# Optimization experiments

Measured on AMD Instinct MI355X. Metric: run time of the kernel, lower is better.

The kernel has to match this reference:

```python
import jax, jax.numpy as jnp
import numpy as np

jax.config.update("jax_enable_x64", True)  # hash uses int64 multiply-xor like torch .long()

NUM_LEVELS = 16
LEVEL_DIM = 2
PER_LEVEL_SCALE = 2
BASE_RES = 16
LOG2_HASHMAP = 19
PS1 = 19349663  # second spatial hash prime (ps[0] == 1)
N_POINTS = 524288


def _isprime(n):
    for p in range(2, int(n ** 0.5) + 1):
        if n % p == 0:
            return False
    return True


N_ENTRIES = 2 ** LOG2_HASHMAP
while not _isprime(N_ENTRIES):
    N_ENTRIES += 1  # -> 524309

SCALES = []
OFFSETS = [0]
START_HASH = NUM_LEVELS  # module uses -1 sentinel; NUM_LEVELS == 'no hashing yet'
for i in range(NUM_LEVELS):
    res = int(BASE_RES * PER_LEVEL_SCALE ** i)
    SCALES.append(res)
    n = (res + 1) ** 2
    if n > N_ENTRIES:
        if START_HASH == NUM_LEVELS:
            START_HASH = i
        n = N_ENTRIES
    OFFSETS.append(OFFSETS[-1] + n)
TABLE_SIZE = OFFSETS[-1]  # 5594552

CORNERS = jnp.array([[0.0, 0.0], [0.0, 1.0], [1.0, 0.0], [1.0, 1.0]], dtype=jnp.float32)  # [4,2]
SCALES_F = jnp.array(SCALES, dtype=jnp.float32)          # [L]
SCALES_I = jnp.array(SCALES, dtype=jnp.int64)            # [L]
LEVEL_OFF = jnp.array(OFFSETS[:-1], dtype=jnp.int64)     # [L] base offset per level


def setup_inputs() -> dict:
    key = jax.random.key(0)
    k1, k2 = jax.random.split(key)
    x = jax.random.uniform(k1, (N_POINTS, 2), dtype=jnp.float32)  # coords in [0,1)
    data = (jax.random.uniform(k2, (TABLE_SIZE, LEVEL_DIM), dtype=jnp.float32) * 2.0 - 1.0) * 1e-4
    return {"x": x, "data": data}


def reference(x, data):
    L, F = NUM_LEVELS, LEVEL_DIM
    float_x = x[None] * SCALES_F[:, None, None]                                  # [L,N,2]
    int_x = (float_x[:, :, None, :] + CORNERS[None, None]).astype(jnp.int64)     # [L,N,4,2]
    offset_x = float_x - int_x[:, :, 0].astype(float_x.dtype)                    # [L,N,2] frac part
    ix0, ix1 = int_x[..., 0], int_x[..., 1]
    # dense-grid index for low levels, spatial hash for high levels
    grid_ind = ix0 * (SCALES_I + 1)[:, None, None] + ix1                         # [L,N,4]
    hash_ind = (ix0 ^ (ix1 * PS1)) % N_ENTRIES                                   # [L,N,4]
    is_grid = (jnp.arange(L) < START_HASH)[:, None, None]
    ind = jnp.where(is_grid, grid_ind, hash_ind) + LEVEL_OFF[:, None, None]      # [L,N,4]
    val = data[ind]                                                              # [L,N,4,F]
    # bilinear corner weights: clamp(1 - c + (2c-1)*frac) per axis, product over xy
    w = jnp.clip(1.0 - CORNERS[None, None] + (2.0 * CORNERS[None, None] - 1.0) * offset_x[:, :, None], 0.0, 1.0)
    w = w[..., 0] * w[..., 1]                                                    # [L,N,4]
    out = jnp.einsum('lnc,lncf->lnf', w, val)                                    # [L,N,F]
    return out.transpose(1, 0, 2).reshape(-1, L * F)                             # [N, L*F]
```

## Files before the change

kernel.cpp:

```cpp
#include <hip/hip_runtime.h>


static constexpr int  kPoints    = 524288;
static constexpr int  kLevels    = 16;
static constexpr int  kStartHash = 6;
static constexpr unsigned kPs1     = 19349663u;
static constexpr unsigned kEntries = 524309u;
static constexpr unsigned kR32     = 352277u;

__constant__ unsigned c_level_off[kLevels] = {
    0u, 289u, 1378u, 5603u, 22244u, 88293u, 351462u,
    875771u, 1400080u, 1924389u, 2448698u, 2973007u,
    3497316u, 4021625u, 4545934u, 5070243u
};

__device__ __forceinline__ float2 interp_level(
    const float2 p, const float2* __restrict__ tbl, const int l)
{
    const int   scale_i = 16 << l;
    const float scale_f = (float)scale_i;

    const float fx = p.x * scale_f;
    const float fy = p.y * scale_f;

    const unsigned ix0 = (unsigned)(int)fx;
    const unsigned iy0 = (unsigned)(int)fy;
    const unsigned ix1 = (unsigned)(int)(fx + 1.0f);
    const unsigned iy1 = (unsigned)(int)(fy + 1.0f);

    const float ox = fx - (float)ix0;
    const float oy = fy - (float)iy0;

    const float wx1 = fminf(fmaxf(ox, 0.0f), 1.0f);
    const float wx0 = fminf(fmaxf(1.0f - ox, 0.0f), 1.0f);
    const float wy1 = fminf(fmaxf(oy, 0.0f), 1.0f);
    const float wy0 = fminf(fmaxf(1.0f - oy, 0.0f), 1.0f);

    unsigned i00, i01, i10, i11;
    if (l < kStartHash) {
        const unsigned stride = (unsigned)(scale_i + 1);
        i00 = ix0 * stride + iy0;
        i01 = ix0 * stride + iy1;
        i10 = ix1 * stride + iy0;
        i11 = ix1 * stride + iy1;
    } else {
        const unsigned long long hy0 = (unsigned long long)iy0 * kPs1;
        const unsigned long long hy1 = (unsigned long long)iy1 * kPs1;
        const unsigned lo0 = (unsigned)hy0, hi0 = (unsigned)(hy0 >> 32);
        const unsigned lo1 = (unsigned)hy1, hi1 = (unsigned)(hy1 >> 32);
        const unsigned a0 = (hi0 * kR32) % kEntries;
        const unsigned a1 = (hi1 * kR32) % kEntries;
        i00 = a0 + ((lo0 ^ ix0) % kEntries); if (i00 >= kEntries) i00 -= kEntries;
        i01 = a1 + ((lo1 ^ ix0) % kEntries); if (i01 >= kEntries) i01 -= kEntries;
        i10 = a0 + ((lo0 ^ ix1) % kEntries); if (i10 >= kEntries) i10 -= kEntries;
        i11 = a1 + ((lo1 ^ ix1) % kEntries); if (i11 >= kEntries) i11 -= kEntries;
    }

    const unsigned base = c_level_off[l];
    const float2 v00 = tbl[base + i00];
    const float2 v01 = tbl[base + i01];
    const float2 v10 = tbl[base + i10];
    const float2 v11 = tbl[base + i11];

    const float w00 = wx0 * wy0;
    const float w01 = wx0 * wy1;
    const float w10 = wx1 * wy0;
    const float w11 = wx1 * wy1;

    return make_float2(
        w00 * v00.x + w01 * v01.x + w10 * v10.x + w11 * v11.x,
        w00 * v00.y + w01 * v01.y + w10 * v10.y + w11 * v11.y);
}

__global__ __launch_bounds__(256) void level_pass(
    const float2* __restrict__ x,
    const float2* __restrict__ tbl,
    float2* __restrict__ ws)
{
    const int b    = blockIdx.x;
    const int xcd  = b & 7;
    const int slot = b >> 3;

    int level, pblk;
    if (slot < 2048) {
        level = 6 + xcd;
        pblk  = slot;
    } else if (slot < 2304) {
        level = 14;
        pblk  = xcd * 256 + (slot - 2048);
    } else if (slot < 2560) {
        level = 15;
        pblk  = xcd * 256 + (slot - 2304);
    } else {
        const int d = xcd * 1536 + (slot - 2560);
        level = d >> 11;
        pblk  = d & 2047;
    }

    const int n = (pblk << 8) | threadIdx.x;
    const float2 p = x[n];
    ws[((size_t)pblk << 12) + (level << 8) + threadIdx.x] =
        interp_level(p, tbl, level);
}

static constexpr int kTStride = 257;

__global__ __launch_bounds__(256) void transpose_out(
    const float2* __restrict__ ws,
    float4* __restrict__ out)
{
    __shared__ float2 lds[kLevels * kTStride];

    const int t = threadIdx.x;
    const float2* __restrict__ tile = ws + ((size_t)blockIdx.x << 12);

#pragma unroll
    for (int l = 0; l < kLevels; ++l)
        lds[l * kTStride + t] = tile[(l << 8) + t];

    __syncthreads();

    float4* o = out + ((size_t)blockIdx.x << 11);
#pragma unroll
    for (int k = 0; k < 8; ++k) {
        const int f  = k * 256 + t;
        const int nl = f >> 3;
        const int i  = t & 7;
        const float2 a = lds[(2 * i)     * kTStride + nl];
        const float2 b = lds[(2 * i + 1) * kTStride + nl];
        o[f] = make_float4(a.x, a.y, b.x, b.y);
    }
}

__global__ __launch_bounds__(256) void hashgrid_fwd(
    const float2* __restrict__ x,
    const float2* __restrict__ tbl,
    float4* __restrict__ out)
{
    const int n = blockIdx.x * blockDim.x + threadIdx.x;
    if (n >= kPoints) return;
    const float2 p = x[n];
    float acc[2 * kLevels];
#pragma unroll
    for (int l = 0; l < kLevels; ++l) {
        const float2 r = interp_level(p, tbl, l);
        acc[2 * l + 0] = r.x;
        acc[2 * l + 1] = r.y;
    }
    float4* o = out + (size_t)n * 8;
#pragma unroll
    for (int i = 0; i < 8; ++i)
        o[i] = make_float4(acc[4 * i + 0], acc[4 * i + 1],
                           acc[4 * i + 2], acc[4 * i + 3]);
}

extern "C" void kernel_launch(void* const* d_in, const int* in_sizes, int n_in,
                              void* d_out, int out_size, void* d_ws, size_t ws_size,
                              hipStream_t stream) {
    const float2* x   = (const float2*)d_in[0];
    const float2* tbl = (const float2*)d_in[1];

    const size_t ws_needed = (size_t)kLevels * kPoints * sizeof(float2);
    if (ws_size >= ws_needed) {
        float2* ws = (float2*)d_ws;
        level_pass<<<kLevels * (kPoints / 256), 256, 0, stream>>>(x, tbl, ws);
        transpose_out<<<kPoints / 256, 256, 0, stream>>>(ws, (float4*)d_out);
    } else {
        hashgrid_fwd<<<kPoints / 256, 256, 0, stream>>>(x, tbl, (float4*)d_out);
    }
}
```

Measured before the change: 222.6 us.

## Process two points per thread in level pass and use nontemporal workspace accesses

Each level_pass thread now handles two points, computing both corner sets before issuing all eight table gathers so more memory loads are in flight per thread, and the grid is halved accordingly with the XCD-to-level mapping rescaled. Workspace writes, workspace reads in the transpose, and the final output stores use nontemporal builtins to keep streaming data from evicting the hash table out of cache. The trade-off is higher register use and fewer blocks, which may reduce occupancy.

```diff
diff --git a/kernel.cpp b/kernel.cpp
--- a/kernel.cpp
+++ b/kernel.cpp
@@ -8,14 +8,34 @@
 static constexpr unsigned kEntries = 524309u;
 static constexpr unsigned kR32     = 352277u;
 
+typedef float v2f __attribute__((ext_vector_type(2)));
+typedef float v4f __attribute__((ext_vector_type(4)));
+
+__device__ __forceinline__ void nt_store2(float2* p, const float2 v) {
+    v2f t; t.x = v.x; t.y = v.y;
+    __builtin_nontemporal_store(t, (v2f*)p);
+}
+__device__ __forceinline__ float2 nt_load2(const float2* p) {
+    const v2f t = __builtin_nontemporal_load((const v2f*)p);
+    return make_float2(t.x, t.y);
+}
+__device__ __forceinline__ void nt_store4(float4* p, const float4 v) {
+    v4f t; t.x = v.x; t.y = v.y; t.z = v.z; t.w = v.w;
+    __builtin_nontemporal_store(t, (v4f*)p);
+}
+
 __constant__ unsigned c_level_off[kLevels] = {
     0u, 289u, 1378u, 5603u, 22244u, 88293u, 351462u,
     875771u, 1400080u, 1924389u, 2448698u, 2973007u,
     3497316u, 4021625u, 4545934u, 5070243u
 };
 
-__device__ __forceinline__ float2 interp_level(
-    const float2 p, const float2* __restrict__ tbl, const int l)
+struct Corners {
+    float    w00, w01, w10, w11;
+    unsigned i00, i01, i10, i11;
+};
+
+__device__ __forceinline__ Corners prep_level(const float2 p, const int l)
 {
     const int   scale_i = 16 << l;
     const float scale_f = (float)scale_i;
@@ -56,20 +76,25 @@
         i11 = a1 + ((lo1 ^ ix1) % kEntries); if (i11 >= kEntries) i11 -= kEntries;
     }
 
+    Corners c;
     const unsigned base = c_level_off[l];
-    const float2 v00 = tbl[base + i00];
-    const float2 v01 = tbl[base + i01];
-    const float2 v10 = tbl[base + i10];
-    const float2 v11 = tbl[base + i11];
-
-    const float w00 = wx0 * wy0;
-    const float w01 = wx0 * wy1;
-    const float w10 = wx1 * wy0;
-    const float w11 = wx1 * wy1;
-
+    c.i00 = base + i00; c.i01 = base + i01;
+    c.i10 = base + i10; c.i11 = base + i11;
+    c.w00 = wx0 * wy0;  c.w01 = wx0 * wy1;
+    c.w10 = wx1 * wy0;  c.w11 = wx1 * wy1;
+    return c;
+}
+
+__device__ __forceinline__ float2 finish_level(
+    const Corners& c, const float2* __restrict__ tbl)
+{
+    const float2 v00 = tbl[c.i00];
+    const float2 v01 = tbl[c.i01];
+    const float2 v10 = tbl[c.i10];
+    const float2 v11 = tbl[c.i11];
     return make_float2(
-        w00 * v00.x + w01 * v01.x + w10 * v10.x + w11 * v11.x,
-        w00 * v00.y + w01 * v01.y + w10 * v10.y + w11 * v11.y);
+        c.w00 * v00.x + c.w01 * v01.x + c.w10 * v10.x + c.w11 * v11.x,
+        c.w00 * v00.y + c.w01 * v01.y + c.w10 * v10.y + c.w11 * v11.y);
 }
 
 __global__ __launch_bounds__(256) void level_pass(
@@ -82,25 +107,44 @@
     const int slot = b >> 3;
 
     int level, pblk;
-    if (slot < 2048) {
+    if (slot < 1024) {
         level = 6 + xcd;
         pblk  = slot;
-    } else if (slot < 2304) {
+    } else if (slot < 1152) {
         level = 14;
-        pblk  = xcd * 256 + (slot - 2048);
-    } else if (slot < 2560) {
+        pblk  = xcd * 128 + (slot - 1024);
+    } else if (slot < 1280) {
         level = 15;
-        pblk  = xcd * 256 + (slot - 2304);
+        pblk  = xcd * 128 + (slot - 1152);
     } else {
-        const int d = xcd * 1536 + (slot - 2560);
-        level = d >> 11;
-        pblk  = d & 2047;
-    }
-
-    const int n = (pblk << 8) | threadIdx.x;
-    const float2 p = x[n];
-    ws[((size_t)pblk << 12) + (level << 8) + threadIdx.x] =
-        interp_level(p, tbl, level);
+        const int d = xcd * 768 + (slot - 1280);
+        level = d >> 10;
+        pblk  = d & 1023;
+    }
+
+    const int n0 = (pblk << 9) | threadIdx.x;
+    const int n1 = n0 + 256;
+    const float2 pA = x[n0];
+    const float2 pB = x[n1];
+
+    const Corners cA = prep_level(pA, level);
+    const Corners cB = prep_level(pB, level);
+
+    const float2 a00 = tbl[cA.i00], a01 = tbl[cA.i01];
+    const float2 a10 = tbl[cA.i10], a11 = tbl[cA.i11];
+    const float2 b00 = tbl[cB.i00], b01 = tbl[cB.i01];
+    const float2 b10 = tbl[cB.i10], b11 = tbl[cB.i11];
+
+    const float2 rA = make_float2(
+        cA.w00 * a00.x + cA.w01 * a01.x + cA.w10 * a10.x + cA.w11 * a11.x,
+        cA.w00 * a00.y + cA.w01 * a01.y + cA.w10 * a10.y + cA.w11 * a11.y);
+    const float2 rB = make_float2(
+        cB.w00 * b00.x + cB.w01 * b01.x + cB.w10 * b10.x + cB.w11 * b11.x,
+        cB.w00 * b00.y + cB.w01 * b01.y + cB.w10 * b10.y + cB.w11 * b11.y);
+
+    const size_t tile0 = (size_t)(n0 >> 8);
+    nt_store2(&ws[(tile0 << 12) + (level << 8) + (n0 & 255)], rA);
+    nt_store2(&ws[((tile0 + 1) << 12) + (level << 8) + (n1 & 255)], rB);
 }
 
 static constexpr int kTStride = 257;
@@ -116,7 +160,7 @@
 
 #pragma unroll
     for (int l = 0; l < kLevels; ++l)
-        lds[l * kTStride + t] = tile[(l << 8) + t];
+        lds[l * kTStride + t] = nt_load2(&tile[(l << 8) + t]);
 
     __syncthreads();
 
@@ -128,7 +172,7 @@
         const int i  = t & 7;
         const float2 a = lds[(2 * i)     * kTStride + nl];
         const float2 b = lds[(2 * i + 1) * kTStride + nl];
-        o[f] = make_float4(a.x, a.y, b.x, b.y);
+        nt_store4(&o[f], make_float4(a.x, a.y, b.x, b.y));
     }
 }
 
@@ -143,7 +187,7 @@
     float acc[2 * kLevels];
 #pragma unroll
     for (int l = 0; l < kLevels; ++l) {
-        const float2 r = interp_level(p, tbl, l);
+        const float2 r = finish_level(prep_level(p, l), tbl);
         acc[2 * l + 0] = r.x;
         acc[2 * l + 1] = r.y;
     }
@@ -163,7 +207,7 @@
     const size_t ws_needed = (size_t)kLevels * kPoints * sizeof(float2);
     if (ws_size >= ws_needed) {
         float2* ws = (float2*)d_ws;
-        level_pass<<<kLevels * (kPoints / 256), 256, 0, stream>>>(x, tbl, ws);
+        level_pass<<<kLevels * (kPoints / 512), 256, 0, stream>>>(x, tbl, ws);
         transpose_out<<<kPoints / 256, 256, 0, stream>>>(ws, (float4*)d_out);
     } else {
         hashgrid_fwd<<<kPoints / 256, 256, 0, stream>>>(x, tbl, (float4*)d_out);
```

After: 237.4 us. 1.07x slower.

## Pair adjacent corner loads into 16-byte reads and split transpose into smaller blocks

Applied to the files above, without the earlier changes.

The level pass splits index/weight prep from the gathers and, when two corner indices are adjacent and 16-byte aligned, fetches both with one 16-byte vector load instead of two 8-byte loads. The transpose kernel now handles 64 points per block, so it launches 4x more blocks with a smaller LDS tile, and it writes output with nontemporal stores. The goal is fewer gather transactions and better transpose occupancy and write behaviour. The cost is a divergent branch per pair and more, smaller blocks.

```diff
diff --git a/kernel.cpp b/kernel.cpp
--- a/kernel.cpp
+++ b/kernel.cpp
@@ -8,14 +8,25 @@
 static constexpr unsigned kEntries = 524309u;
 static constexpr unsigned kR32     = 352277u;
 
+typedef float v4f __attribute__((ext_vector_type(4)));
+
+__device__ __forceinline__ void nt_store4(float4* p, const float4 v) {
+    v4f t; t.x = v.x; t.y = v.y; t.z = v.z; t.w = v.w;
+    __builtin_nontemporal_store(t, (v4f*)p);
+}
+
 __constant__ unsigned c_level_off[kLevels] = {
     0u, 289u, 1378u, 5603u, 22244u, 88293u, 351462u,
     875771u, 1400080u, 1924389u, 2448698u, 2973007u,
     3497316u, 4021625u, 4545934u, 5070243u
 };
 
-__device__ __forceinline__ float2 interp_level(
-    const float2 p, const float2* __restrict__ tbl, const int l)
+struct Corners {
+    float    w00, w01, w10, w11;
+    unsigned i00, i01, i10, i11;
+};
+
+__device__ __forceinline__ Corners prep_level(const float2 p, const int l)
 {
     const int   scale_i = 16 << l;
     const float scale_f = (float)scale_i;
@@ -56,20 +67,27 @@
         i11 = a1 + ((lo1 ^ ix1) % kEntries); if (i11 >= kEntries) i11 -= kEntries;
     }
 
+    Corners c;
     const unsigned base = c_level_off[l];
-    const float2 v00 = tbl[base + i00];
-    const float2 v01 = tbl[base + i01];
-    const float2 v10 = tbl[base + i10];
-    const float2 v11 = tbl[base + i11];
-
-    const float w00 = wx0 * wy0;
-    const float w01 = wx0 * wy1;
-    const float w10 = wx1 * wy0;
-    const float w11 = wx1 * wy1;
-
-    return make_float2(
-        w00 * v00.x + w01 * v01.x + w10 * v10.x + w11 * v11.x,
-        w00 * v00.y + w01 * v01.y + w10 * v10.y + w11 * v11.y);
+    c.i00 = base + i00; c.i01 = base + i01;
+    c.i10 = base + i10; c.i11 = base + i11;
+    c.w00 = wx0 * wy0;  c.w01 = wx0 * wy1;
+    c.w10 = wx1 * wy0;  c.w11 = wx1 * wy1;
+    return c;
+}
+
+__device__ __forceinline__ void load_pair(
+    const float2* __restrict__ tbl, const unsigned ia, const unsigned ib,
+    float2& va, float2& vb)
+{
+    if (ib == ia + 1u && !(ia & 1u)) {
+        const v4f q = *reinterpret_cast<const v4f*>(&tbl[ia]);
+        va = make_float2(q.x, q.y);
+        vb = make_float2(q.z, q.w);
+    } else {
+        va = tbl[ia];
+        vb = tbl[ib];
+    }
 }
 
 __global__ __launch_bounds__(256) void level_pass(
@@ -99,36 +117,57 @@
 
     const int n = (pblk << 8) | threadIdx.x;
     const float2 p = x[n];
-    ws[((size_t)pblk << 12) + (level << 8) + threadIdx.x] =
-        interp_level(p, tbl, level);
-}
-
-static constexpr int kTStride = 257;
+    const Corners c = prep_level(p, level);
+
+    float2 v00, v01, v10, v11;
+    if (level < kStartHash) {
+        load_pair(tbl, c.i00, c.i01, v00, v01);
+        load_pair(tbl, c.i10, c.i11, v10, v11);
+    } else {
+        load_pair(tbl, c.i00, c.i10, v00, v10);
+        load_pair(tbl, c.i01, c.i11, v01, v11);
+    }
+
+    const float2 r = make_float2(
+        c.w00 * v00.x + c.w01 * v01.x + c.w10 * v10.x + c.w11 * v11.x,
+        c.w00 * v00.y + c.w01 * v01.y + c.w10 * v10.y + c.w11 * v11.y);
+
+    ws[((size_t)pblk << 12) + (level << 8) + threadIdx.x] = r;
+}
+
+static constexpr int kT2S = 66;
 
 __global__ __launch_bounds__(256) void transpose_out(
     const float2* __restrict__ ws,
     float4* __restrict__ out)
 {
-    __shared__ float2 lds[kLevels * kTStride];
+    __shared__ float2 lds[kLevels][kT2S];
 
     const int t = threadIdx.x;
-    const float2* __restrict__ tile = ws + ((size_t)blockIdx.x << 12);
-
-#pragma unroll
-    for (int l = 0; l < kLevels; ++l)
-        lds[l * kTStride + t] = tile[(l << 8) + t];
+    const int b = blockIdx.x;
+    const int chunk = b >> 2;
+    const int coff  = (b & 3) << 6;
+    const float2* __restrict__ base = ws + ((size_t)chunk << 12) + coff;
+
+#pragma unroll
+    for (int k = 0; k < 4; ++k) {
+        const int e = (k << 8) + t;
+        const int l = e >> 6;
+        const int cc = e & 63;
+        lds[l][cc] = base[(l << 8) + cc];
+    }
 
     __syncthreads();
 
-    float4* o = out + ((size_t)blockIdx.x << 11);
-#pragma unroll
-    for (int k = 0; k < 8; ++k) {
-        const int f  = k * 256 + t;
-        const int nl = f >> 3;
-        const int i  = t & 7;
-        const float2 a = lds[(2 * i)     * kTStride + nl];
-        const float2 b = lds[(2 * i + 1) * kTStride + nl];
-        o[f] = make_float4(a.x, a.y, b.x, b.y);
+    float4* o = out + ((size_t)b << 9);
+#pragma unroll
+    for (int k = 0; k < 2; ++k) {
+        const int g  = (k << 8) + t;
+        const int nl = g >> 3;
+        const int i  = g & 7;
+        const float2 a  = lds[2 * i][nl];
+        const float2 bb = lds[2 * i + 1][nl];
+        nt_store4(&o[g], make_float4(a.x, a.y, bb.x, bb.y));
     }
 }
 
@@ -143,9 +182,11 @@
     float acc[2 * kLevels];
 #pragma unroll
     for (int l = 0; l < kLevels; ++l) {
-        const float2 r = interp_level(p, tbl, l);
-        acc[2 * l + 0] = r.x;
-        acc[2 * l + 1] = r.y;
+        const Corners c = prep_level(p, l);
+        const float2 v00 = tbl[c.i00], v01 = tbl[c.i01];
+        const float2 v10 = tbl[c.i10], v11 = tbl[c.i11];
+        acc[2 * l + 0] = c.w00 * v00.x + c.w01 * v01.x + c.w10 * v10.x + c.w11 * v11.x;
+        acc[2 * l + 1] = c.w00 * v00.y + c.w01 * v01.y + c.w10 * v10.y + c.w11 * v11.y;
     }
     float4* o = out + (size_t)n * 8;
 #pragma unroll
@@ -164,7 +205,7 @@
     if (ws_size >= ws_needed) {
         float2* ws = (float2*)d_ws;
         level_pass<<<kLevels * (kPoints / 256), 256, 0, stream>>>(x, tbl, ws);
-        transpose_out<<<kPoints / 256, 256, 0, stream>>>(ws, (float4*)d_out);
+        transpose_out<<<kPoints / 64, 256, 0, stream>>>(ws, (float4*)d_out);
     } else {
         hashgrid_fwd<<<kPoints / 256, 256, 0, stream>>>(x, tbl, (float4*)d_out);
     }
```

New measurement: 211.8 us. 1.05x faster.
